# Kernel optimization log

Measured on AMD Instinct MI355X. Metric: run time of the kernel, lower is better.

Reference implementation:

```python
import jax, jax.numpy as jnp
import numpy as np

B, T, TREF, NBINS, H = 4096, 8192, 8192, 50, 32  # np.linspace(lo,hi,50) -> 49 bins
EPS = 1e-10


def setup_inputs() -> dict:
    key = jax.random.key(0)
    k0, k1, k2, k3, k4, k5 = jax.random.split(key, 6)
    return {
        "current_returns": jax.random.normal(k0, (B, T), jnp.float32) * 0.02,
        "reference_returns": jax.random.normal(k1, (TREF,), jnp.float32) * 0.02,
        "w1": jax.random.normal(k2, (H, 1), jnp.float32) * 0.5,   # Linear(1, H).weight
        "b1": jax.random.normal(k3, (H,), jnp.float32) * 0.1,
        "w2": jax.random.normal(k4, (H, H), jnp.float32) * 0.1,   # Linear(H, H).weight
        "b2": jax.random.normal(k5, (H,), jnp.float32) * 0.1,
    }


def _kl_from_hists(ref, curr, ref_min, ref_max):
    # Faithful to InformationTheory.kl_divergence with n_bins=50 (49 equal-width bins).
    nb = NBINS - 1
    lo = jnp.minimum(ref_min, curr.min())
    hi = jnp.maximum(ref_max, curr.max())
    width = (hi - lo) / nb

    def hist_density(x):
        # np.histogram(x, bins=linspace(lo,hi,50), density=True); all x in [lo,hi],
        # right edge goes to last bin (handled by clip).
        idx = jnp.clip(jnp.floor((x - lo) / width).astype(jnp.int32), 0, nb - 1)
        counts = jnp.zeros(nb, jnp.float32).at[idx].add(1.0)
        return counts / (x.shape[0] * width)

    p = hist_density(ref) + EPS
    q = hist_density(curr) + EPS
    p = p / p.sum()
    q = q / q.sum()
    return jnp.sum(p * jnp.log(p / q))


def reference(current_returns, reference_returns, w1, b1, w2, b2):
    ref = reference_returns
    ref_min, ref_max = ref.min(), ref.max()
    kl = jax.vmap(lambda c: _kl_from_hists(ref, c, ref_min, ref_max))(current_returns)  # [B]
    kl = jax.lax.stop_gradient(kl)  # original detaches before building kl_tensor
    x = kl[:, None]                                  # [B, 1]
    h = jax.nn.relu(x @ w1.T + b1)                   # [B, H]
    encoded = h @ w2.T + b2                          # [B, H]
    return kl, encoded
```

## Files before the change

### kernel.cpp

```cpp
#include <hip/hip_runtime.h>
#include <math.h>

constexpr int T_LEN  = 8192;
constexpr int B_ROWS = 4096;
constexpr int NB     = 49;
constexpr int NC     = 32;
constexpr int HDIM   = 32;
constexpr int FBINS  = 8192;
constexpr float EPSF = 1e-10f;

constexpr int WS_CDF_OFF    = 8;
constexpr int WS_BINNED_OFF = 8208;

#define HP(i) ((i) + ((i) >> 5))

__device__ __forceinline__ void lds_fence() {
    asm volatile("s_waitcnt lgkmcnt(0)" ::: "memory");
    __builtin_amdgcn_sched_barrier(0);
}

__global__ __launch_bounds__(256)
void ref_cdf_kernel(const float* __restrict__ ref, float* __restrict__ wsf) {
    __shared__ float sv[FBINS];
    __shared__ int   hist[HP(FBINS)];
    __shared__ int   wsum[4];
    __shared__ float rmn4[4], rmx4[4];
    const int tid  = threadIdx.x;
    const int lane = tid & 63;
    const int wave = tid >> 6;

    const float4* r4 = (const float4*)ref;
    float4* sv4 = (float4*)sv;
    float mn = 3.0e38f, mx = -3.0e38f;
    #pragma unroll
    for (int i = 0; i < 8; ++i) {
        float4 v = r4[tid + i * 256];
        sv4[tid + i * 256] = v;
        mn = fminf(mn, fminf(fminf(v.x, v.y), fminf(v.z, v.w)));
        mx = fmaxf(mx, fmaxf(fmaxf(v.x, v.y), fmaxf(v.z, v.w)));
    }
    for (int i = tid; i < HP(FBINS); i += 256) hist[i] = 0;
    #pragma unroll
    for (int off = 32; off > 0; off >>= 1) {
        mn = fminf(mn, __shfl_xor(mn, off));
        mx = fmaxf(mx, __shfl_xor(mx, off));
    }
    if (lane == 0) { rmn4[wave] = mn; rmx4[wave] = mx; }
    __syncthreads();
    const float rmin = fminf(fminf(rmn4[0], rmn4[1]), fminf(rmn4[2], rmn4[3]));
    const float rmax = fmaxf(fmaxf(rmx4[0], rmx4[1]), fmaxf(rmx4[2], rmx4[3]));
    const float finv = (float)FBINS / (rmax - rmin);

    for (int i = tid; i < FBINS; i += 256) {
        int fb = min(max((int)((sv[i] - rmin) * finv), 0), FBINS - 1);
        atomicAdd(&hist[HP(fb)], 1);
    }
    __syncthreads();

    const int base = tid * 32;
    int s = 0;
    #pragma unroll
    for (int j = 0; j < 32; ++j) {
        int h = hist[HP(base + j)]; hist[HP(base + j)] = s; s += h;
    }
    const int own = s;
    int incl = s;
    #pragma unroll
    for (int off = 1; off < 64; off <<= 1) {
        int t = __shfl_up(incl, off);
        if (lane >= off) incl += t;
    }
    if (lane == 63) wsum[wave] = incl;
    __syncthreads();
    int woff = 0;
    #pragma unroll
    for (int w = 0; w < 4; ++w) if (w < wave) woff += wsum[w];
    const int add = woff + incl - own;
    #pragma unroll
    for (int j = 0; j < 32; ++j) hist[HP(base + j)] += add;
    __syncthreads();

    int* cdf = (int*)(wsf + WS_CDF_OFF);
    for (int i = tid; i < FBINS; i += 256) cdf[i] = hist[HP(i)];
    if (tid == 0) { cdf[FBINS] = T_LEN; wsf[0] = rmin; wsf[1] = rmax; }
    __syncthreads();

    float* binned = wsf + WS_BINNED_OFF;
    for (int i = tid; i < FBINS; i += 256) {
        float x = sv[i];
        int fb = min(max((int)((x - rmin) * finv), 0), FBINS - 1);
        int pos = atomicAdd(&hist[HP(fb)], 1);
        binned[pos] = x;
    }
}

__global__ __launch_bounds__(64, 3)
void kl_wave_kernel(const float* __restrict__ cur,
                    const float* __restrict__ wsf,
                    const float* __restrict__ w1,
                    const float* __restrict__ b1,
                    const float* __restrict__ w2,
                    const float* __restrict__ b2,
                    float* __restrict__ kl_out,
                    float* __restrict__ enc_out) {
    __shared__ unsigned hq[NC * NB];

    const int lane = threadIdx.x;
    const int b    = blockIdx.x;
    const float4* src = (const float4*)(cur + (size_t)b * T_LEN);

    float4 v[32];
    #pragma unroll
    for (int i = 0; i < 32; ++i) v[i] = src[lane + i * 64];

    #pragma unroll
    for (int i = 0; i < 25; ++i) {
        int idx = lane + i * 64;
        if (idx < NC * NB) hq[idx] = 0u;
    }
    const float rmin = wsf[0], rmax = wsf[1];

    float mn = 3.0e38f, mx = -3.0e38f;
    #pragma unroll
    for (int i = 0; i < 32; ++i) {
        mn = fminf(mn, fminf(fminf(v[i].x, v[i].y), fminf(v[i].z, v[i].w)));
        mx = fmaxf(mx, fmaxf(fmaxf(v[i].x, v[i].y), fmaxf(v[i].z, v[i].w)));
    }
    #pragma unroll
    for (int off = 32; off > 0; off >>= 1) {
        mn = fminf(mn, __shfl_xor(mn, off));
        mx = fmaxf(mx, __shfl_xor(mx, off));
    }
    const float lo = fminf(rmin, mn);
    const float hi = fmaxf(rmax, mx);
    const float width = (hi - lo) / (float)NB;
    const float winv = 1.0f / width, nlw = -lo * winv;

    lds_fence();
    unsigned* myq = hq + (lane & (NC - 1)) * NB;
    #pragma unroll
    for (int i = 0; i < 32; ++i) {
        int i0 = min(max((int)fmaf(v[i].x, winv, nlw), 0), NB - 1);
        int i1 = min(max((int)fmaf(v[i].y, winv, nlw), 0), NB - 1);
        int i2 = min(max((int)fmaf(v[i].z, winv, nlw), 0), NB - 1);
        int i3 = min(max((int)fmaf(v[i].w, winv, nlw), 0), NB - 1);
        atomicAdd(&myq[i0], 1u); atomicAdd(&myq[i1], 1u);
        atomicAdd(&myq[i2], 1u); atomicAdd(&myq[i3], 1u);
    }
    lds_fence();

    const bool act = lane < NB;
    const float inv = 1.0f / ((float)T_LEN * width);
    float p = 0.0f, q = 0.0f;
    if (act) {
        unsigned sq = 0u;
        #pragma unroll
        for (int c = 0; c < NC; ++c) sq += hq[c * NB + lane];
        q = (float)sq * inv + EPSF;
    }
    int C = T_LEN;
    if (lane < NB - 1) {
        const float kp1  = (float)(lane + 1);
        const float finv = (float)FBINS / (rmax - rmin);
        const int* cdf = (const int*)(wsf + WS_CDF_OFF);
        const float* binned = wsf + WS_BINNED_OFF;
        const float t = fmaf(width, kp1, lo);
        int fb = (int)floorf((t - rmin) * finv);
        int a  = min(max(fb - 2, 0), FBINS);
        int bb = min(max(fb + 3, 0), FBINS);
        int ia = cdf[a], ib = cdf[bb];
        C = ia;
        for (int i = ia; i < ib; i += 4) {
            float x0 = binned[i];
            float x1 = (i + 1 < ib) ? binned[i + 1] : 3.0e38f;
            float x2 = (i + 2 < ib) ? binned[i + 2] : 3.0e38f;
            float x3 = (i + 3 < ib) ? binned[i + 3] : 3.0e38f;
            C += ((x0 - lo) / width < kp1) ? 1 : 0;
            C += ((x1 - lo) / width < kp1) ? 1 : 0;
            C += ((x2 - lo) / width < kp1) ? 1 : 0;
            C += ((x3 - lo) / width < kp1) ? 1 : 0;
        }
    }
    int Cprev = __shfl_up(C, 1);
    if (lane == 0) Cprev = 0;
    if (act) p = (float)(C - Cprev) * inv + EPSF;

    float P = p, Q = q;
    #pragma unroll
    for (int off = 32; off > 0; off >>= 1) {
        P += __shfl_xor(P, off);
        Q += __shfl_xor(Q, off);
    }
    float term = 0.0f;
    if (act) {
        const float pn = p / P;
        const float qn = q / Q;
        term = pn * logf(pn / qn);
    }
    #pragma unroll
    for (int off = 32; off > 0; off >>= 1) term += __shfl_xor(term, off);
    if (lane == 0) kl_out[b] = term;

    if (lane < HDIM) {
        float acc = b2[lane];
        #pragma unroll
        for (int t2 = 0; t2 < HDIM; ++t2) {
            float h = fmaxf(fmaf(term, w1[t2], b1[t2]), 0.0f);
            acc = fmaf(h, w2[lane * HDIM + t2], acc);
        }
        enc_out[(size_t)b * HDIM + lane] = acc;
    }
}

extern "C" void kernel_launch(void* const* d_in, const int* in_sizes, int n_in,
                              void* d_out, int out_size, void* d_ws, size_t ws_size,
                              hipStream_t stream) {
    const float* cur = (const float*)d_in[0];
    const float* ref = (const float*)d_in[1];
    const float* w1  = (const float*)d_in[2];
    const float* b1  = (const float*)d_in[3];
    const float* w2  = (const float*)d_in[4];
    const float* b2  = (const float*)d_in[5];
    float* out = (float*)d_out;
    float* wsf = (float*)d_ws;

    ref_cdf_kernel<<<1, 256, 0, stream>>>(ref, wsf);
    kl_wave_kernel<<<B_ROWS, 64, 0, stream>>>(
        cur, wsf, w1, b1, w2, b2, out, out + B_ROWS);
}
```

Baseline: 44.14 us.

## Process each row with a 256-thread block staging data via direct global-to-LDS loads

Each row is now handled by a 4-wave block instead of a single wave. The row is loaded asynchronously into LDS with global_load_lds, and min/max and histogram binning are split across all 256 threads, with a block-level reduction through shared memory. Only the first wave does the reference-CDF lookup, the KL term and the MLP. The intent is more memory-level parallelism and less register pressure than the 32-float4-per-lane design. In exchange, each block uses 32KB of LDS, which limits occupancy, and adds block-wide barriers. The lower clamp on bin indices is also dropped.

```diff
diff --git a/kernel.cpp b/kernel.cpp
--- a/kernel.cpp
+++ b/kernel.cpp
@@ -14,8 +14,9 @@
 
 #define HP(i) ((i) + ((i) >> 5))
 
-__device__ __forceinline__ void lds_fence() {
+__device__ __forceinline__ void sync_lds() {
     asm volatile("s_waitcnt lgkmcnt(0)" ::: "memory");
+    __builtin_amdgcn_s_barrier();
     __builtin_amdgcn_sched_barrier(0);
 }
 
@@ -94,121 +95,135 @@
     }
 }
 
-__global__ __launch_bounds__(64, 3)
-void kl_wave_kernel(const float* __restrict__ cur,
-                    const float* __restrict__ wsf,
-                    const float* __restrict__ w1,
-                    const float* __restrict__ b1,
-                    const float* __restrict__ w2,
-                    const float* __restrict__ b2,
-                    float* __restrict__ kl_out,
-                    float* __restrict__ enc_out) {
+__global__ __launch_bounds__(256, 4)
+void kl_lds_kernel(const float* __restrict__ cur,
+                   const float* __restrict__ wsf,
+                   const float* __restrict__ w1,
+                   const float* __restrict__ b1,
+                   const float* __restrict__ w2,
+                   const float* __restrict__ b2,
+                   float* __restrict__ kl_out,
+                   float* __restrict__ enc_out) {
+    __shared__ float row[T_LEN];
     __shared__ unsigned hq[NC * NB];
-
-    const int lane = threadIdx.x;
+    __shared__ float rmnS[4], rmxS[4];
+
+    const int tid  = threadIdx.x;
+    const int lane = tid & 63;
+    const int wave = tid >> 6;
     const int b    = blockIdx.x;
-    const float4* src = (const float4*)(cur + (size_t)b * T_LEN);
-
-    float4 v[32];
-    #pragma unroll
-    for (int i = 0; i < 32; ++i) v[i] = src[lane + i * 64];
-
-    #pragma unroll
-    for (int i = 0; i < 25; ++i) {
-        int idx = lane + i * 64;
-        if (idx < NC * NB) hq[idx] = 0u;
-    }
+    const float* src = cur + (size_t)b * T_LEN;
+
+    #pragma unroll
+    for (int i = 0; i < 8; ++i) {
+        const float* g = src + wave * 2048 + i * 256 + lane * 4;
+        __builtin_amdgcn_global_load_lds(
+            (const __attribute__((address_space(1))) void*)g,
+            (__attribute__((address_space(3))) void*)&row[wave * 2048 + i * 256],
+            16, 0, 0);
+    }
+    for (int i = tid; i < NC * NB; i += 256) hq[i] = 0u;
     const float rmin = wsf[0], rmax = wsf[1];
-
+    __syncthreads();
+
+    const float4* row4 = (const float4*)row;
     float mn = 3.0e38f, mx = -3.0e38f;
     #pragma unroll
-    for (int i = 0; i < 32; ++i) {
-        mn = fminf(mn, fminf(fminf(v[i].x, v[i].y), fminf(v[i].z, v[i].w)));
-        mx = fmaxf(mx, fmaxf(fmaxf(v[i].x, v[i].y), fmaxf(v[i].z, v[i].w)));
+    for (int i = 0; i < 8; ++i) {
+        float4 t = row4[tid + i * 256];
+        mn = fminf(mn, fminf(fminf(t.x, t.y), fminf(t.z, t.w)));
+        mx = fmaxf(mx, fmaxf(fmaxf(t.x, t.y), fmaxf(t.z, t.w)));
     }
     #pragma unroll
     for (int off = 32; off > 0; off >>= 1) {
         mn = fminf(mn, __shfl_xor(mn, off));
         mx = fmaxf(mx, __shfl_xor(mx, off));
     }
-    const float lo = fminf(rmin, mn);
-    const float hi = fmaxf(rmax, mx);
+    if (lane == 0) { rmnS[wave] = mn; rmxS[wave] = mx; }
+    sync_lds();
+
+    const float lo = fminf(rmin,
+        fminf(fminf(rmnS[0], rmnS[1]), fminf(rmnS[2], rmnS[3])));
+    const float hi = fmaxf(rmax,
+        fmaxf(fmaxf(rmxS[0], rmxS[1]), fmaxf(rmxS[2], rmxS[3])));
     const float width = (hi - lo) / (float)NB;
     const float winv = 1.0f / width, nlw = -lo * winv;
 
-    lds_fence();
-    unsigned* myq = hq + (lane & (NC - 1)) * NB;
-    #pragma unroll
-    for (int i = 0; i < 32; ++i) {
-        int i0 = min(max((int)fmaf(v[i].x, winv, nlw), 0), NB - 1);
-        int i1 = min(max((int)fmaf(v[i].y, winv, nlw), 0), NB - 1);
-        int i2 = min(max((int)fmaf(v[i].z, winv, nlw), 0), NB - 1);
-        int i3 = min(max((int)fmaf(v[i].w, winv, nlw), 0), NB - 1);
+    unsigned* myq = hq + (tid & (NC - 1)) * NB;
+    #pragma unroll
+    for (int i = 0; i < 8; ++i) {
+        float4 t = row4[tid + i * 256];
+        int i0 = min((int)fmaf(t.x, winv, nlw), NB - 1);
+        int i1 = min((int)fmaf(t.y, winv, nlw), NB - 1);
+        int i2 = min((int)fmaf(t.z, winv, nlw), NB - 1);
+        int i3 = min((int)fmaf(t.w, winv, nlw), NB - 1);
         atomicAdd(&myq[i0], 1u); atomicAdd(&myq[i1], 1u);
         atomicAdd(&myq[i2], 1u); atomicAdd(&myq[i3], 1u);
     }
-    lds_fence();
-
-    const bool act = lane < NB;
-    const float inv = 1.0f / ((float)T_LEN * width);
-    float p = 0.0f, q = 0.0f;
-    if (act) {
-        unsigned sq = 0u;
+    sync_lds();
+
+    if (tid < 64) {
+        const bool act = lane < NB;
+        const float inv = 1.0f / ((float)T_LEN * width);
+        float p = 0.0f, q = 0.0f;
+        if (act) {
+            unsigned sq = 0u;
+            #pragma unroll
+            for (int c = 0; c < NC; ++c) sq += hq[c * NB + lane];
+            q = (float)sq * inv + EPSF;
+        }
+        int C = T_LEN;
+        if (lane < NB - 1) {
+            const float kp1  = (float)(lane + 1);
+            const float finv = (float)FBINS / (rmax - rmin);
+            const int* cdf = (const int*)(wsf + WS_CDF_OFF);
+            const float* binned = wsf + WS_BINNED_OFF;
+            const float t = fmaf(width, kp1, lo);
+            int fb = (int)floorf((t - rmin) * finv);
+            int a  = min(max(fb - 2, 0), FBINS);
+            int bb = min(max(fb + 3, 0), FBINS);
+            int ia = cdf[a], ib = cdf[bb];
+            C = ia;
+            for (int i = ia; i < ib; i += 4) {
+                float x0 = binned[i];
+                float x1 = (i + 1 < ib) ? binned[i + 1] : 3.0e38f;
+                float x2 = (i + 2 < ib) ? binned[i + 2] : 3.0e38f;
+                float x3 = (i + 3 < ib) ? binned[i + 3] : 3.0e38f;
+                C += ((x0 - lo) / width < kp1) ? 1 : 0;
+                C += ((x1 - lo) / width < kp1) ? 1 : 0;
+                C += ((x2 - lo) / width < kp1) ? 1 : 0;
+                C += ((x3 - lo) / width < kp1) ? 1 : 0;
+            }
+        }
+        int Cprev = __shfl_up(C, 1);
+        if (lane == 0) Cprev = 0;
+        if (act) p = (float)(C - Cprev) * inv + EPSF;
+
+        float P = p, Q = q;
         #pragma unroll
-        for (int c = 0; c < NC; ++c) sq += hq[c * NB + lane];
-        q = (float)sq * inv + EPSF;
-    }
-    int C = T_LEN;
-    if (lane < NB - 1) {
-        const float kp1  = (float)(lane + 1);
-        const float finv = (float)FBINS / (rmax - rmin);
-        const int* cdf = (const int*)(wsf + WS_CDF_OFF);
-        const float* binned = wsf + WS_BINNED_OFF;
-        const float t = fmaf(width, kp1, lo);
-        int fb = (int)floorf((t - rmin) * finv);
-        int a  = min(max(fb - 2, 0), FBINS);
-        int bb = min(max(fb + 3, 0), FBINS);
-        int ia = cdf[a], ib = cdf[bb];
-        C = ia;
-        for (int i = ia; i < ib; i += 4) {
-            float x0 = binned[i];
-            float x1 = (i + 1 < ib) ? binned[i + 1] : 3.0e38f;
-            float x2 = (i + 2 < ib) ? binned[i + 2] : 3.0e38f;
-            float x3 = (i + 3 < ib) ? binned[i + 3] : 3.0e38f;
-            C += ((x0 - lo) / width < kp1) ? 1 : 0;
-            C += ((x1 - lo) / width < kp1) ? 1 : 0;
-            C += ((x2 - lo) / width < kp1) ? 1 : 0;
-            C += ((x3 - lo) / width < kp1) ? 1 : 0;
-        }
-    }
-    int Cprev = __shfl_up(C, 1);
-    if (lane == 0) Cprev = 0;
-    if (act) p = (float)(C - Cprev) * inv + EPSF;
-
-    float P = p, Q = q;
-    #pragma unroll
-    for (int off = 32; off > 0; off >>= 1) {
-        P += __shfl_xor(P, off);
-        Q += __shfl_xor(Q, off);
-    }
-    float term = 0.0f;
-    if (act) {
-        const float pn = p / P;
-        const float qn = q / Q;
-        term = pn * logf(pn / qn);
-    }
-    #pragma unroll
-    for (int off = 32; off > 0; off >>= 1) term += __shfl_xor(term, off);
-    if (lane == 0) kl_out[b] = term;
-
-    if (lane < HDIM) {
-        float acc = b2[lane];
+        for (int off = 32; off > 0; off >>= 1) {
+            P += __shfl_xor(P, off);
+            Q += __shfl_xor(Q, off);
+        }
+        float term = 0.0f;
+        if (act) {
+            const float pn = p / P;
+            const float qn = q / Q;
+            term = pn * logf(pn / qn);
+        }
         #pragma unroll
-        for (int t2 = 0; t2 < HDIM; ++t2) {
-            float h = fmaxf(fmaf(term, w1[t2], b1[t2]), 0.0f);
-            acc = fmaf(h, w2[lane * HDIM + t2], acc);
-        }
-        enc_out[(size_t)b * HDIM + lane] = acc;
+        for (int off = 32; off > 0; off >>= 1) term += __shfl_xor(term, off);
+        if (lane == 0) kl_out[b] = term;
+
+        if (lane < HDIM) {
+            float acc = b2[lane];
+            #pragma unroll
+            for (int t2 = 0; t2 < HDIM; ++t2) {
+                float h = fmaxf(fmaf(term, w1[t2], b1[t2]), 0.0f);
+                acc = fmaf(h, w2[lane * HDIM + t2], acc);
+            }
+            enc_out[(size_t)b * HDIM + lane] = acc;
+        }
     }
 }
 
@@ -225,6 +240,6 @@
     float* wsf = (float*)d_ws;
 
     ref_cdf_kernel<<<1, 256, 0, stream>>>(ref, wsf);
-    kl_wave_kernel<<<B_ROWS, 64, 0, stream>>>(
+    kl_lds_kernel<<<B_ROWS, 256, 0, stream>>>(
         cur, wsf, w1, b1, w2, b2, out, out + B_ROWS);
 }
```

Measured after the change: 47.55 us. 1.08x slower.

## Split per-row binning from KL and MLP tail into separate kernels

Applied to the files above, without the earlier changes.

The single per-row wave kernel becomes two kernels. A streaming binning kernel only builds each row's 49-bin histogram and writes the counts plus lo and width to a workspace record. A separate 256-thread tail kernel, one wave per row, reads those records and does the reference-CDF search, the KL reduction and the small MLP. The aim is to keep the latency-heavy CDF lookup and MLP out of the bandwidth-bound pass, and the binning loop also drops the lower clamp and one LDS fence. The cost is an extra kernel launch and a small global round trip for the records, and dropping the clamp relies on the bin index never being negative.

```diff
diff --git a/kernel.cpp b/kernel.cpp
--- a/kernel.cpp
+++ b/kernel.cpp
@@ -7,10 +7,12 @@
 constexpr int NC     = 32;
 constexpr int HDIM   = 32;
 constexpr int FBINS  = 8192;
+constexpr int RECW   = 52;
 constexpr float EPSF = 1e-10f;
 
 constexpr int WS_CDF_OFF    = 8;
 constexpr int WS_BINNED_OFF = 8208;
+constexpr int WS_QREC_OFF   = 16400;
 
 #define HP(i) ((i) + ((i) >> 5))
 
@@ -95,14 +97,9 @@
 }
 
 __global__ __launch_bounds__(64, 3)
-void kl_wave_kernel(const float* __restrict__ cur,
-                    const float* __restrict__ wsf,
-                    const float* __restrict__ w1,
-                    const float* __restrict__ b1,
-                    const float* __restrict__ w2,
-                    const float* __restrict__ b2,
-                    float* __restrict__ kl_out,
-                    float* __restrict__ enc_out) {
+void bin_wave_kernel(const float* __restrict__ cur,
+                     const float* __restrict__ wsf,
+                     float* __restrict__ qrec) {
     __shared__ unsigned hq[NC * NB];
 
     const int lane = threadIdx.x;
@@ -136,28 +133,50 @@
     const float width = (hi - lo) / (float)NB;
     const float winv = 1.0f / width, nlw = -lo * winv;
 
-    lds_fence();
     unsigned* myq = hq + (lane & (NC - 1)) * NB;
     #pragma unroll
     for (int i = 0; i < 32; ++i) {
-        int i0 = min(max((int)fmaf(v[i].x, winv, nlw), 0), NB - 1);
-        int i1 = min(max((int)fmaf(v[i].y, winv, nlw), 0), NB - 1);
-        int i2 = min(max((int)fmaf(v[i].z, winv, nlw), 0), NB - 1);
-        int i3 = min(max((int)fmaf(v[i].w, winv, nlw), 0), NB - 1);
+        int i0 = min((int)fmaf(v[i].x, winv, nlw), NB - 1);
+        int i1 = min((int)fmaf(v[i].y, winv, nlw), NB - 1);
+        int i2 = min((int)fmaf(v[i].z, winv, nlw), NB - 1);
+        int i3 = min((int)fmaf(v[i].w, winv, nlw), NB - 1);
         atomicAdd(&myq[i0], 1u); atomicAdd(&myq[i1], 1u);
         atomicAdd(&myq[i2], 1u); atomicAdd(&myq[i3], 1u);
     }
     lds_fence();
 
+    float* rec = qrec + (size_t)b * RECW;
+    if (lane < NB) {
+        unsigned sq = 0u;
+        #pragma unroll
+        for (int c = 0; c < NC; ++c) sq += hq[c * NB + lane];
+        rec[lane] = (float)sq;
+    }
+    if (lane == NB)     rec[NB]     = lo;
+    if (lane == NB + 1) rec[NB + 1] = width;
+}
+
+__global__ __launch_bounds__(256)
+void tail_kernel(const float* __restrict__ wsf,
+                 const float* __restrict__ qrec,
+                 const float* __restrict__ w1,
+                 const float* __restrict__ b1,
+                 const float* __restrict__ w2,
+                 const float* __restrict__ b2,
+                 float* __restrict__ kl_out,
+                 float* __restrict__ enc_out) {
+    const int lane = threadIdx.x & 63;
+    const int wave = threadIdx.x >> 6;
+    const int row  = blockIdx.x * 4 + wave;
+    const float* rec = qrec + (size_t)row * RECW;
+
+    const float rmin = wsf[0], rmax = wsf[1];
+    const float lo = rec[NB], width = rec[NB + 1];
     const bool act = lane < NB;
     const float inv = 1.0f / ((float)T_LEN * width);
     float p = 0.0f, q = 0.0f;
-    if (act) {
-        unsigned sq = 0u;
-        #pragma unroll
-        for (int c = 0; c < NC; ++c) sq += hq[c * NB + lane];
-        q = (float)sq * inv + EPSF;
-    }
+    if (act) q = rec[lane] * inv + EPSF;
+
     int C = T_LEN;
     if (lane < NB - 1) {
         const float kp1  = (float)(lane + 1);
@@ -199,7 +218,7 @@
     }
     #pragma unroll
     for (int off = 32; off > 0; off >>= 1) term += __shfl_xor(term, off);
-    if (lane == 0) kl_out[b] = term;
+    if (lane == 0) kl_out[row] = term;
 
     if (lane < HDIM) {
         float acc = b2[lane];
@@ -208,7 +227,7 @@
             float h = fmaxf(fmaf(term, w1[t2], b1[t2]), 0.0f);
             acc = fmaf(h, w2[lane * HDIM + t2], acc);
         }
-        enc_out[(size_t)b * HDIM + lane] = acc;
+        enc_out[(size_t)row * HDIM + lane] = acc;
     }
 }
 
@@ -221,10 +240,12 @@
     const float* b1  = (const float*)d_in[3];
     const float* w2  = (const float*)d_in[4];
     const float* b2  = (const float*)d_in[5];
-    float* out = (float*)d_out;
-    float* wsf = (float*)d_ws;
+    float* out  = (float*)d_out;
+    float* wsf  = (float*)d_ws;
+    float* qrec = wsf + WS_QREC_OFF;
 
     ref_cdf_kernel<<<1, 256, 0, stream>>>(ref, wsf);
-    kl_wave_kernel<<<B_ROWS, 64, 0, stream>>>(
-        cur, wsf, w1, b1, w2, b2, out, out + B_ROWS);
-}
+    bin_wave_kernel<<<B_ROWS, 64, 0, stream>>>(cur, wsf, qrec);
+    tail_kernel<<<B_ROWS / 4, 256, 0, stream>>>(
+        wsf, qrec, w1, b1, w2, b2, out, out + B_ROWS);
+}
```

New measurement: 47.18 us. +6.9%, slower.
